# Performance work log

Hardware: AMD Instinct MI355X
Metric: run time of the kernel (lower is better)

The kernel has to match this reference:

```python
import jax, jax.numpy as jnp
import numpy as np

B, K, H, L = 50000, 32, 128, 64
KL_BETA = 0.001
LN_EPS = 1e-5


def _layernorm(x, g, b):
    m = jnp.mean(x, axis=-1, keepdims=True)
    v = jnp.mean((x - m) ** 2, axis=-1, keepdims=True)
    return (x - m) * jax.lax.rsqrt(v + LN_EPS) * g + b


def setup_inputs() -> dict:
    key = jax.random.key(0)
    ks = jax.random.split(key, 16)
    s = 0.05
    return {
        "self_feat": jax.random.normal(ks[0], (B, H), jnp.float32),
        "neighbor_feat": jax.random.normal(ks[1], (B, K, H), jnp.float32),
        "trust_mask": jax.random.uniform(ks[2], (B, K, 1), jnp.float32),
        "eps": jax.random.normal(ks[3], (B, K, L), jnp.float32),
        "pre_g": jnp.ones((H,), jnp.float32), "pre_b": jnp.zeros((H,), jnp.float32),
        "W_mu": jax.random.normal(ks[4], (H, L), jnp.float32) * s, "b_mu": jnp.zeros((L,), jnp.float32),
        "W_lv": jax.random.normal(ks[5], (H, L), jnp.float32) * s, "b_lv": jnp.zeros((L,), jnp.float32),
        "post_g": jnp.ones((L,), jnp.float32), "post_b": jnp.zeros((L,), jnp.float32),
        "W_q": jax.random.normal(ks[6], (H, L), jnp.float32) * s, "b_q": jnp.zeros((L,), jnp.float32),
        "W_k": jax.random.normal(ks[7], (L, L), jnp.float32) * s, "b_k": jnp.zeros((L,), jnp.float32),
        "W_v": jax.random.normal(ks[8], (L, L), jnp.float32) * s, "b_v": jnp.zeros((L,), jnp.float32),
        "W_o": jax.random.normal(ks[9], (L, H), jnp.float32) * s, "b_o": jnp.zeros((H,), jnp.float32),
    }


def reference(self_feat, neighbor_feat, trust_mask, eps,
              pre_g, pre_b, W_mu, b_mu, W_lv, b_lv, post_g, post_b,
              W_q, b_q, W_k, b_k, W_v, b_v, W_o, b_o):
    # [B,K,H] -> layernorm -> VIB reparameterization -> [B,K,L]
    nn = _layernorm(neighbor_feat, pre_g, pre_b)
    mu = nn @ W_mu + b_mu                      # [B,K,L]
    logvar = nn @ W_lv + b_lv                  # [B,K,L]
    z = mu + eps * jnp.exp(0.5 * logvar)       # reparam
    z = _layernorm(z, post_g, post_b)
    # trust-masked single-query attention over K neighbors
    q = self_feat @ W_q + b_q                  # [B,L]
    k = z @ W_k + b_k                          # [B,K,L]
    v = z @ W_v + b_v                          # [B,K,L]
    logits = jnp.einsum("bl,bkl->bk", q, k) / jnp.sqrt(jnp.float32(L))
    logits = logits + jnp.log(trust_mask[..., 0] + 1e-6)
    attn = jax.nn.softmax(logits, axis=-1)     # [B,K]
    context = jnp.einsum("bk,bkl->bl", attn, v)
    comm_feat = context @ W_o + b_o            # [B,H]
    kl = -0.5 * jnp.mean(jnp.sum(1.0 + logvar - mu ** 2 - jnp.exp(logvar), axis=-1))
    return comm_feat, KL_BETA * kl
```

## Files before the change

kernel.cpp:

```cpp
#include <hip/hip_runtime.h>
#include <hip/hip_bf16.h>

typedef float f32x4 __attribute__((ext_vector_type(4)));
typedef short bf16x8 __attribute__((ext_vector_type(8)));

#define NB 50000
#define NK 32
#define NH 128
#define NL 64

static __device__ __forceinline__ unsigned short f2bf(float f) {
    unsigned int u = __float_as_uint(f);
    u += 0x7fffu + ((u >> 16) & 1u);
    return (unsigned short)(u >> 16);
}
static __device__ __forceinline__ float bf2f(unsigned short u) {
    return __uint_as_float(((unsigned int)u) << 16);
}
static __device__ __forceinline__ float bflo(unsigned int u) { return __uint_as_float(u << 16); }
static __device__ __forceinline__ float bfhi(unsigned int u) { return __uint_as_float(u & 0xffff0000u); }

__global__ void kl_zero_kernel(float* out) {
    if (threadIdx.x == 0 && blockIdx.x == 0) out[(size_t)NB * NH] = 0.0f;
}

__global__ void __launch_bounds__(256) wvo_kernel(const float* __restrict__ W_v,
                                                  const float* __restrict__ W_o,
                                                  const float* __restrict__ b_v,
                                                  const float* __restrict__ b_o,
                                                  float* __restrict__ wvo_ws,
                                                  float* __restrict__ bvo_ws)
{
    const int t = threadIdx.x;
    for (int e = t; e < 64 * 128; e += 256) {
        int d = e >> 7, h = e & 127;
        float s = 0.f;
#pragma unroll 8
        for (int c = 0; c < 64; ++c) s += W_v[d * 64 + c] * W_o[c * 128 + h];
        wvo_ws[e] = s;
    }
    if (t < 128) {
        float s = b_o[t];
#pragma unroll 8
        for (int c = 0; c < 64; ++c) s += b_v[c] * W_o[c * 128 + t];
        bvo_ws[t] = s;
    }
}

__global__ void __launch_bounds__(256) qk_kernel(const float* __restrict__ self_feat,
                                                 const float* __restrict__ W_q,
                                                 const float* __restrict__ b_q,
                                                 const float* __restrict__ W_k,
                                                 float* __restrict__ qk_ws)
{
    __shared__ __align__(16) unsigned short A[32 * 128];
    __shared__ __align__(16) unsigned short ZQ[32 * 64];
    const int t = threadIdx.x, w = t >> 6, l = t & 63, g = l >> 4, li = l & 15;

    bf16x8 Bq[4];
#pragma unroll
    for (int s = 0; s < 4; ++s) {
        int k0 = 32 * s + 8 * g, c = li + 16 * w;
        bf16x8 f;
#pragma unroll
        for (int j = 0; j < 8; ++j) f[j] = (short)f2bf(W_q[(k0 + j) * 64 + c]);
        Bq[s] = f;
    }
    bf16x8 Bk[2];
#pragma unroll
    for (int s = 0; s < 2; ++s) {
        int k0 = 32 * s + 8 * g, d = li + 16 * w;
        bf16x8 f;
#pragma unroll
        for (int j = 0; j < 8; ++j) f[j] = (short)f2bf(W_k[d * 64 + k0 + j]);
        Bk[s] = f;
    }
    const float bq = b_q[li + 16 * w];
    const int n0 = blockIdx.x * 32;

    {
        int row = t >> 3, c0 = (t & 7) * 16;
        float x[16];
        if (n0 + row < NB) {
            const float* src = self_feat + (size_t)(n0 + row) * NH + c0;
#pragma unroll
            for (int i = 0; i < 4; ++i) {
                float4 v4 = ((const float4*)src)[i];
                x[4 * i] = v4.x; x[4 * i + 1] = v4.y; x[4 * i + 2] = v4.z; x[4 * i + 3] = v4.w;
            }
        } else {
#pragma unroll
            for (int i = 0; i < 16; ++i) x[i] = 0.f;
        }
        alignas(16) unsigned short yb[16];
#pragma unroll
        for (int i = 0; i < 16; ++i) yb[i] = f2bf(x[i]);
        int boff = row * 256 + c0 * 2;
        *(int4*)((char*)A + ((boff) ^ ((row & 7) << 4))) = *(int4*)&yb[0];
        *(int4*)((char*)A + ((boff + 16) ^ ((row & 7) << 4))) = *(int4*)&yb[8];
    }
    __syncthreads();

    const f32x4 zero4 = {0.f, 0.f, 0.f, 0.f};
    f32x4 acc[2] = {zero4, zero4};
#pragma unroll
    for (int s = 0; s < 4; ++s) {
        bf16x8 A0 = *(const bf16x8*)((const char*)A + ((li * 256 + s * 64 + g * 16) ^ ((li & 7) << 4)));
        bf16x8 A1 = *(const bf16x8*)((const char*)A + (((16 + li) * 256 + s * 64 + g * 16) ^ ((li & 7) << 4)));
        acc[0] = __builtin_amdgcn_mfma_f32_16x16x32_bf16(A0, Bq[s], acc[0], 0, 0, 0);
        acc[1] = __builtin_amdgcn_mfma_f32_16x16x32_bf16(A1, Bq[s], acc[1], 0, 0, 0);
    }
#pragma unroll
    for (int mt = 0; mt < 2; ++mt)
#pragma unroll
        for (int r = 0; r < 4; ++r) {
            int row = 16 * mt + 4 * g + r, c = li + 16 * w;
            *(unsigned short*)((char*)ZQ + ((row * 128 + c * 2) ^ ((row & 7) << 4))) = f2bf(acc[mt][r] + bq);
        }
    __syncthreads();

    f32x4 acc2[2] = {zero4, zero4};
#pragma unroll
    for (int s = 0; s < 2; ++s) {
        bf16x8 A0 = *(const bf16x8*)((const char*)ZQ + ((li * 128 + s * 64 + g * 16) ^ ((li & 7) << 4)));
        bf16x8 A1 = *(const bf16x8*)((const char*)ZQ + (((16 + li) * 128 + s * 64 + g * 16) ^ (((16 + li) & 7) << 4)));
        acc2[0] = __builtin_amdgcn_mfma_f32_16x16x32_bf16(A0, Bk[s], acc2[0], 0, 0, 0);
        acc2[1] = __builtin_amdgcn_mfma_f32_16x16x32_bf16(A1, Bk[s], acc2[1], 0, 0, 0);
    }
#pragma unroll
    for (int mt = 0; mt < 2; ++mt)
#pragma unroll
        for (int r = 0; r < 4; ++r) {
            int row = 16 * mt + 4 * g + r;
            if (n0 + row < NB)
                qk_ws[(size_t)(n0 + row) * 64 + li + 16 * w] = acc2[mt][r];
        }
}

__global__ void __launch_bounds__(256) fz10_kernel(
    const float* __restrict__ neighbor_feat, const float* __restrict__ trust_mask,
    const float* __restrict__ eps_g,
    const float* __restrict__ pre_g, const float* __restrict__ pre_b,
    const float* __restrict__ W_mu, const float* __restrict__ b_mu,
    const float* __restrict__ W_lv, const float* __restrict__ b_lv,
    const float* __restrict__ post_g, const float* __restrict__ post_b,
    const float* __restrict__ qk_ws, const float* __restrict__ wvo_ws,
    const float* __restrict__ bvo_ws,
    float* __restrict__ out)
{
    __shared__ __align__(16) unsigned short A[32 * 128];
    __shared__ float muv[128 * 33];
    __shared__ float2 s_pgb[128];
    __shared__ float s_bmu[64], s_blv[64], s_pg[64], s_pb[64];
    __shared__ float logit_l[32];
    __shared__ float zpart[4][64];
    __shared__ float klw[4];

    const int t = threadIdx.x, w = t >> 6, l = t & 63, g = l >> 4, li = l & 15;

    if (t < 128) s_pgb[t] = make_float2(pre_g[t], pre_b[t]);
    if (t < 64) { s_bmu[t] = b_mu[t]; s_blv[t] = b_lv[t]; s_pg[t] = post_g[t]; s_pb[t] = post_b[t]; }

    bf16x8 Wml[2][4];
    {
        const float* Wsrc = (w < 2) ? W_mu : W_lv;
        int cb = 32 * (w & 1) + li;
#pragma unroll
        for (int ntp = 0; ntp < 2; ++ntp)
#pragma unroll
            for (int s = 0; s < 4; ++s) {
                int k0 = 32 * s + 8 * g, c = cb + 16 * ntp;
                bf16x8 f;
#pragma unroll
                for (int j = 0; j < 8; ++j) f[j] = (short)f2bf(Wsrc[(k0 + j) * 64 + c]);
                Wml[ntp][s] = f;
            }
    }
    const int h = 32 * w + (l & 31);
    const int chalf = l >> 5;
    unsigned int wvo_pk[16];
#pragma unroll
    for (int j = 0; j < 16; ++j) {
        int c = 32 * chalf + 2 * j;
        wvo_pk[j] = (unsigned)f2bf(wvo_ws[c * 128 + h]) | ((unsigned)f2bf(wvo_ws[(c + 1) * 128 + h]) << 16);
    }
    const float bvo_r = bvo_ws[h];
    __syncthreads();

    const int row = t >> 3;
    const int c0 = (t & 7) * 16;
    const int l0 = (t & 7) * 8;
    int bn = blockIdx.x * 8;

    float x[16], ee[8], qk8[8], trr;
    {
        const float* src = neighbor_feat + ((size_t)bn * NK + row) * NH + c0;
#pragma unroll
        for (int i = 0; i < 4; ++i) {
            float4 v4 = ((const float4*)src)[i];
            x[4 * i] = v4.x; x[4 * i + 1] = v4.y; x[4 * i + 2] = v4.z; x[4 * i + 3] = v4.w;
        }
        const float* ep = eps_g + ((size_t)bn * NK + row) * NL + l0;
        float4 e0 = ((const float4*)ep)[0], e1 = ((const float4*)ep)[1];
        ee[0] = e0.x; ee[1] = e0.y; ee[2] = e0.z; ee[3] = e0.w;
        ee[4] = e1.x; ee[5] = e1.y; ee[6] = e1.z; ee[7] = e1.w;
        const float* qp = qk_ws + (size_t)bn * 64 + l0;
        float4 q0 = ((const float4*)qp)[0], q1 = ((const float4*)qp)[1];
        qk8[0] = q0.x; qk8[1] = q0.y; qk8[2] = q0.z; qk8[3] = q0.w;
        qk8[4] = q1.x; qk8[5] = q1.y; qk8[6] = q1.z; qk8[7] = q1.w;
        trr = trust_mask[(size_t)bn * NK + row];
    }

    float kl_acc = 0.f;
    const f32x4 zero4 = {0.f, 0.f, 0.f, 0.f};

#pragma unroll 1
    for (int i = 0; i < 8; ++i, ++bn) {
        const int bnx = (i < 7) ? bn + 1 : bn;

        float s1 = 0.f;
#pragma unroll
        for (int j = 0; j < 16; ++j) s1 += x[j];
        s1 += __shfl_xor(s1, 1); s1 += __shfl_xor(s1, 2); s1 += __shfl_xor(s1, 4);
        float mean = s1 * (1.f / 128.f);
        float s2 = 0.f;
#pragma unroll
        for (int j = 0; j < 16; ++j) { float d = x[j] - mean; s2 += d * d; }
        s2 += __shfl_xor(s2, 1); s2 += __shfl_xor(s2, 2); s2 += __shfl_xor(s2, 4);
        float inv = rsqrtf(s2 * (1.f / 128.f) + 1e-5f);
        alignas(16) unsigned short yb[16];
#pragma unroll
        for (int j = 0; j < 16; ++j) {
            float2 gb = s_pgb[c0 + j];
            yb[j] = f2bf((x[j] - mean) * inv * gb.x + gb.y);
        }
        {
            int boff = row * 256 + c0 * 2;
            *(int4*)((char*)A + ((boff) ^ ((row & 7) << 4))) = *(int4*)&yb[0];
            *(int4*)((char*)A + ((boff + 16) ^ ((row & 7) << 4))) = *(int4*)&yb[8];
        }
        {
            const float* src = neighbor_feat + ((size_t)bnx * NK + row) * NH + c0;
#pragma unroll
            for (int j = 0; j < 4; ++j) {
                float4 v4 = ((const float4*)src)[j];
                x[4 * j] = v4.x; x[4 * j + 1] = v4.y; x[4 * j + 2] = v4.z; x[4 * j + 3] = v4.w;
            }
        }
        __syncthreads();

        {
            f32x4 acc[2][2];
            acc[0][0] = zero4; acc[0][1] = zero4; acc[1][0] = zero4; acc[1][1] = zero4;
#pragma unroll
            for (int s = 0; s < 4; ++s) {
                bf16x8 A0 = *(const bf16x8*)((const char*)A + ((li * 256 + s * 64 + g * 16) ^ ((li & 7) << 4)));
                bf16x8 A1 = *(const bf16x8*)((const char*)A + (((16 + li) * 256 + s * 64 + g * 16) ^ ((li & 7) << 4)));
#pragma unroll
                for (int ntp = 0; ntp < 2; ++ntp) {
                    acc[0][ntp] = __builtin_amdgcn_mfma_f32_16x16x32_bf16(A0, Wml[ntp][s], acc[0][ntp], 0, 0, 0);
                    acc[1][ntp] = __builtin_amdgcn_mfma_f32_16x16x32_bf16(A1, Wml[ntp][s], acc[1][ntp], 0, 0, 0);
                }
            }
#pragma unroll
            for (int mt = 0; mt < 2; ++mt)
#pragma unroll
                for (int ntp = 0; ntp < 2; ++ntp)
#pragma unroll
                    for (int r = 0; r < 4; ++r)
                        muv[(32 * w + 16 * ntp + li) * 33 + (16 * mt + 4 * g + r)] = acc[mt][ntp][r];
        }
        __syncthreads();

        float zr[8];
#pragma unroll
        for (int j = 0; j < 8; ++j) {
            float mu = muv[(l0 + j) * 33 + row] + s_bmu[l0 + j];
            float lv = muv[(64 + l0 + j) * 33 + row] + s_blv[l0 + j];
            float eh = __expf(0.5f * lv);
            kl_acc += 1.f + lv - mu * mu - eh * eh;
            zr[j] = mu + ee[j] * eh;
        }
        {
            const float* ep = eps_g + ((size_t)bnx * NK + row) * NL + l0;
            float4 e0 = ((const float4*)ep)[0], e1 = ((const float4*)ep)[1];
            ee[0] = e0.x; ee[1] = e0.y; ee[2] = e0.z; ee[3] = e0.w;
            ee[4] = e1.x; ee[5] = e1.y; ee[6] = e1.z; ee[7] = e1.w;
        }
        {
            float zs = 0.f;
#pragma unroll
            for (int j = 0; j < 8; ++j) zs += zr[j];
            zs += __shfl_xor(zs, 1); zs += __shfl_xor(zs, 2); zs += __shfl_xor(zs, 4);
            float zm = zs * (1.f / 64.f);
            float zv = 0.f;
#pragma unroll
            for (int j = 0; j < 8; ++j) { float d = zr[j] - zm; zv += d * d; }
            zv += __shfl_xor(zv, 1); zv += __shfl_xor(zv, 2); zv += __shfl_xor(zv, 4);
            float zi = rsqrtf(zv * (1.f / 64.f) + 1e-5f);
#pragma unroll
            for (int j = 0; j < 8; ++j)
                zr[j] = (zr[j] - zm) * zi * s_pg[l0 + j] + s_pb[l0 + j];
        }
        {
            float lg = 0.f;
#pragma unroll
            for (int j = 0; j < 8; ++j) lg += zr[j] * qk8[j];
            lg += __shfl_xor(lg, 1); lg += __shfl_xor(lg, 2); lg += __shfl_xor(lg, 4);
            if ((t & 7) == 0) logit_l[row] = lg * 0.125f + __logf(trr + 1e-6f);
        }
        {
            const float* qp = qk_ws + (size_t)bnx * 64 + l0;
            float4 q0 = ((const float4*)qp)[0], q1 = ((const float4*)qp)[1];
            qk8[0] = q0.x; qk8[1] = q0.y; qk8[2] = q0.z; qk8[3] = q0.w;
            qk8[4] = q1.x; qk8[5] = q1.y; qk8[6] = q1.z; qk8[7] = q1.w;
            trr = trust_mask[(size_t)bnx * NK + row];
        }
        __syncthreads();

        {
            float lgv = logit_l[l & 31];
            float mx = lgv;
            mx = fmaxf(mx, __shfl_xor(mx, 1));  mx = fmaxf(mx, __shfl_xor(mx, 2));
            mx = fmaxf(mx, __shfl_xor(mx, 4));  mx = fmaxf(mx, __shfl_xor(mx, 8));
            mx = fmaxf(mx, __shfl_xor(mx, 16));
            float ev = __expf(lgv - mx);
            float den = ev;
            den += __shfl_xor(den, 1); den += __shfl_xor(den, 2);
            den += __shfl_xor(den, 4); den += __shfl_xor(den, 8);
            den += __shfl_xor(den, 16);
            float att_own = __expf(logit_l[row] - mx) / den;
            float av[8];
#pragma unroll
            for (int j = 0; j < 8; ++j) av[j] = att_own * zr[j];
#pragma unroll
            for (int j = 0; j < 8; ++j) {
                av[j] += __shfl_xor(av[j], 8);
                av[j] += __shfl_xor(av[j], 16);
                av[j] += __shfl_xor(av[j], 32);
            }
            if (l < 8) {
                float4 p0 = {av[0], av[1], av[2], av[3]};
                float4 p1 = {av[4], av[5], av[6], av[7]};
                ((float4*)&zpart[w][8 * l])[0] = p0;
                ((float4*)&zpart[w][8 * l])[1] = p1;
            }
        }
        __syncthreads();

        {
            float o = 0.f;
#pragma unroll
            for (int j = 0; j < 16; ++j) {
                int c = 32 * chalf + 2 * j;
                float2 z0 = *(const float2*)&zpart[0][c];
                float2 z1 = *(const float2*)&zpart[1][c];
                float2 z2 = *(const float2*)&zpart[2][c];
                float2 z3 = *(const float2*)&zpart[3][c];
                float zs0 = z0.x + z1.x + z2.x + z3.x;
                float zs1 = z0.y + z1.y + z2.y + z3.y;
                o += zs0 * bflo(wvo_pk[j]) + zs1 * bfhi(wvo_pk[j]);
            }
            o += __shfl_xor(o, 32);
            if (l < 32) out[(size_t)bn * NH + h] = o + bvo_r;
        }
    }

#pragma unroll
    for (int msk = 1; msk < 64; msk <<= 1) kl_acc += __shfl_xor(kl_acc, msk);
    if (l == 0) klw[w] = kl_acc;
    __syncthreads();
    if (t == 0) {
        float tot = klw[0] + klw[1] + klw[2] + klw[3];
        atomicAdd(out + (size_t)NB * NH, tot * (-0.5f * 0.001f / ((float)NB * NK)));
    }
}

extern "C" void kernel_launch(void* const* d_in, const int* in_sizes, int n_in,
                              void* d_out, int out_size, void* d_ws, size_t ws_size,
                              hipStream_t stream) {
    const float* self_feat     = (const float*)d_in[0];
    const float* neighbor_feat = (const float*)d_in[1];
    const float* trust_mask    = (const float*)d_in[2];
    const float* eps           = (const float*)d_in[3];
    const float* pre_g  = (const float*)d_in[4];
    const float* pre_b  = (const float*)d_in[5];
    const float* W_mu   = (const float*)d_in[6];
    const float* b_mu   = (const float*)d_in[7];
    const float* W_lv   = (const float*)d_in[8];
    const float* b_lv   = (const float*)d_in[9];
    const float* post_g = (const float*)d_in[10];
    const float* post_b = (const float*)d_in[11];
    const float* W_q    = (const float*)d_in[12];
    const float* b_q    = (const float*)d_in[13];
    const float* W_k    = (const float*)d_in[14];
    const float* W_v    = (const float*)d_in[16];
    const float* b_v    = (const float*)d_in[17];
    const float* W_o    = (const float*)d_in[18];
    const float* b_o    = (const float*)d_in[19];
    float* out = (float*)d_out;

    float* qk_ws  = (float*)d_ws;
    float* wvo_ws = qk_ws + (size_t)NB * 64;
    float* bvo_ws = wvo_ws + 64 * 128;

    hipLaunchKernelGGL(kl_zero_kernel, dim3(1), dim3(64), 0, stream, out);
    hipLaunchKernelGGL(wvo_kernel, dim3(1), dim3(256), 0, stream, W_v, W_o, b_v, b_o, wvo_ws, bvo_ws);
    hipLaunchKernelGGL(qk_kernel, dim3((NB + 31) / 32), dim3(256), 0, stream,
                       self_feat, W_q, b_q, W_k, qk_ws);
    hipLaunchKernelGGL(fz10_kernel, dim3(NB / 8), dim3(256), 0, stream,
                       neighbor_feat, trust_mask, eps, pre_g, pre_b,
                       W_mu, b_mu, W_lv, b_lv, post_g, post_b,
                       qk_ws, wvo_ws, bvo_ws, out);
}
```

Before: 522.1 us.

## Batch output projection across 8 rows via MFMA and reorganize muv layout

The per-row output projection (context @ W_vo) with its extra __syncthreads per iteration is replaced by accumulating all 8 rows' context vectors in shared memory and doing one batched MFMA at the end. A split hi/lo bf16 trick keeps the activations near fp32 precision. The muv shared buffer is transposed to a row-major layout with 132 padding, and the lane-to-column mapping switches from contiguous to strided so eps/qk loads become scalar and strided. This removes one barrier per loop iteration but wastes half the MFMA rows and makes the eps/qk global loads less vectorized.

```diff
diff --git a/kernel.cpp b/kernel.cpp
--- a/kernel.cpp
+++ b/kernel.cpp
@@ -17,8 +17,6 @@
 static __device__ __forceinline__ float bf2f(unsigned short u) {
     return __uint_as_float(((unsigned int)u) << 16);
 }
-static __device__ __forceinline__ float bflo(unsigned int u) { return __uint_as_float(u << 16); }
-static __device__ __forceinline__ float bfhi(unsigned int u) { return __uint_as_float(u & 0xffff0000u); }
 
 __global__ void kl_zero_kernel(float* out) {
     if (threadIdx.x == 0 && blockIdx.x == 0) out[(size_t)NB * NH] = 0.0f;
@@ -137,7 +135,7 @@
         }
 }
 
-__global__ void __launch_bounds__(256) fz10_kernel(
+__global__ void __launch_bounds__(256) fz11_kernel(
     const float* __restrict__ neighbor_feat, const float* __restrict__ trust_mask,
     const float* __restrict__ eps_g,
     const float* __restrict__ pre_g, const float* __restrict__ pre_b,
@@ -149,11 +147,11 @@
     float* __restrict__ out)
 {
     __shared__ __align__(16) unsigned short A[32 * 128];
-    __shared__ float muv[128 * 33];
+    __shared__ float muv[32 * 132];
+    __shared__ float zparts[8][4][64];
     __shared__ float2 s_pgb[128];
     __shared__ float s_bmu[64], s_blv[64], s_pg[64], s_pb[64];
     __shared__ float logit_l[32];
-    __shared__ float zpart[4][64];
     __shared__ float klw[4];
 
     const int t = threadIdx.x, w = t >> 6, l = t & 63, g = l >> 4, li = l & 15;
@@ -176,21 +174,25 @@
                 Wml[ntp][s] = f;
             }
     }
-    const int h = 32 * w + (l & 31);
-    const int chalf = l >> 5;
-    unsigned int wvo_pk[16];
-#pragma unroll
-    for (int j = 0; j < 16; ++j) {
-        int c = 32 * chalf + 2 * j;
-        wvo_pk[j] = (unsigned)f2bf(wvo_ws[c * 128 + h]) | ((unsigned)f2bf(wvo_ws[(c + 1) * 128 + h]) << 16);
-    }
-    const float bvo_r = bvo_ws[h];
+    bf16x8 Bvo[2][2];
+#pragma unroll
+    for (int nt = 0; nt < 2; ++nt)
+#pragma unroll
+        for (int s = 0; s < 2; ++s) {
+            int k0 = 32 * s + 8 * g, c = 32 * w + 16 * nt + li;
+            bf16x8 f;
+#pragma unroll
+            for (int j = 0; j < 8; ++j) f[j] = (short)f2bf(wvo_ws[(k0 + j) * 128 + c]);
+            Bvo[nt][s] = f;
+        }
+    const float bvo2[2] = { bvo_ws[32 * w + li], bvo_ws[32 * w + 16 + li] };
     __syncthreads();
 
     const int row = t >> 3;
     const int c0 = (t & 7) * 16;
-    const int l0 = (t & 7) * 8;
-    int bn = blockIdx.x * 8;
+    const int a  = t & 7;
+    const int bn0 = blockIdx.x * 8;
+    int bn = bn0;
 
     float x[16], ee[8], qk8[8], trr;
     {
@@ -200,14 +202,10 @@
             float4 v4 = ((const float4*)src)[i];
             x[4 * i] = v4.x; x[4 * i + 1] = v4.y; x[4 * i + 2] = v4.z; x[4 * i + 3] = v4.w;
         }
-        const float* ep = eps_g + ((size_t)bn * NK + row) * NL + l0;
-        float4 e0 = ((const float4*)ep)[0], e1 = ((const float4*)ep)[1];
-        ee[0] = e0.x; ee[1] = e0.y; ee[2] = e0.z; ee[3] = e0.w;
-        ee[4] = e1.x; ee[5] = e1.y; ee[6] = e1.z; ee[7] = e1.w;
-        const float* qp = qk_ws + (size_t)bn * 64 + l0;
-        float4 q0 = ((const float4*)qp)[0], q1 = ((const float4*)qp)[1];
-        qk8[0] = q0.x; qk8[1] = q0.y; qk8[2] = q0.z; qk8[3] = q0.w;
-        qk8[4] = q1.x; qk8[5] = q1.y; qk8[6] = q1.z; qk8[7] = q1.w;
+        const float* ep = eps_g + ((size_t)bn * NK + row) * NL;
+        const float* qp = qk_ws + (size_t)bn * 64;
+#pragma unroll
+        for (int j = 0; j < 8; ++j) { ee[j] = ep[a + 8 * j]; qk8[j] = qp[a + 8 * j]; }
         trr = trust_mask[(size_t)bn * NK + row];
     }
 
@@ -268,24 +266,24 @@
                 for (int ntp = 0; ntp < 2; ++ntp)
 #pragma unroll
                     for (int r = 0; r < 4; ++r)
-                        muv[(32 * w + 16 * ntp + li) * 33 + (16 * mt + 4 * g + r)] = acc[mt][ntp][r];
+                        muv[(16 * mt + 4 * g + r) * 132 + 32 * w + 16 * ntp + li] = acc[mt][ntp][r];
         }
         __syncthreads();
 
         float zr[8];
 #pragma unroll
         for (int j = 0; j < 8; ++j) {
-            float mu = muv[(l0 + j) * 33 + row] + s_bmu[l0 + j];
-            float lv = muv[(64 + l0 + j) * 33 + row] + s_blv[l0 + j];
+            int c = a + 8 * j;
+            float mu = muv[row * 132 + c] + s_bmu[c];
+            float lv = muv[row * 132 + 64 + c] + s_blv[c];
             float eh = __expf(0.5f * lv);
             kl_acc += 1.f + lv - mu * mu - eh * eh;
             zr[j] = mu + ee[j] * eh;
         }
         {
-            const float* ep = eps_g + ((size_t)bnx * NK + row) * NL + l0;
-            float4 e0 = ((const float4*)ep)[0], e1 = ((const float4*)ep)[1];
-            ee[0] = e0.x; ee[1] = e0.y; ee[2] = e0.z; ee[3] = e0.w;
-            ee[4] = e1.x; ee[5] = e1.y; ee[6] = e1.z; ee[7] = e1.w;
+            const float* ep = eps_g + ((size_t)bnx * NK + row) * NL;
+#pragma unroll
+            for (int j = 0; j < 8; ++j) ee[j] = ep[a + 8 * j];
         }
         {
             float zs = 0.f;
@@ -299,21 +297,22 @@
             zv += __shfl_xor(zv, 1); zv += __shfl_xor(zv, 2); zv += __shfl_xor(zv, 4);
             float zi = rsqrtf(zv * (1.f / 64.f) + 1e-5f);
 #pragma unroll
-            for (int j = 0; j < 8; ++j)
-                zr[j] = (zr[j] - zm) * zi * s_pg[l0 + j] + s_pb[l0 + j];
+            for (int j = 0; j < 8; ++j) {
+                int c = a + 8 * j;
+                zr[j] = (zr[j] - zm) * zi * s_pg[c] + s_pb[c];
+            }
         }
         {
             float lg = 0.f;
 #pragma unroll
             for (int j = 0; j < 8; ++j) lg += zr[j] * qk8[j];
             lg += __shfl_xor(lg, 1); lg += __shfl_xor(lg, 2); lg += __shfl_xor(lg, 4);
-            if ((t & 7) == 0) logit_l[row] = lg * 0.125f + __logf(trr + 1e-6f);
-        }
-        {
-            const float* qp = qk_ws + (size_t)bnx * 64 + l0;
-            float4 q0 = ((const float4*)qp)[0], q1 = ((const float4*)qp)[1];
-            qk8[0] = q0.x; qk8[1] = q0.y; qk8[2] = q0.z; qk8[3] = q0.w;
-            qk8[4] = q1.x; qk8[5] = q1.y; qk8[6] = q1.z; qk8[7] = q1.w;
+            if (a == 0) logit_l[row] = lg * 0.125f + __logf(trr + 1e-6f);
+        }
+        {
+            const float* qp = qk_ws + (size_t)bnx * 64;
+#pragma unroll
+            for (int j = 0; j < 8; ++j) qk8[j] = qp[a + 8 * j];
             trr = trust_mask[(size_t)bnx * NK + row];
         }
         __syncthreads();
@@ -340,30 +339,44 @@
                 av[j] += __shfl_xor(av[j], 32);
             }
             if (l < 8) {
-                float4 p0 = {av[0], av[1], av[2], av[3]};
-                float4 p1 = {av[4], av[5], av[6], av[7]};
-                ((float4*)&zpart[w][8 * l])[0] = p0;
-                ((float4*)&zpart[w][8 * l])[1] = p1;
-            }
-        }
-        __syncthreads();
-
-        {
-            float o = 0.f;
-#pragma unroll
-            for (int j = 0; j < 16; ++j) {
-                int c = 32 * chalf + 2 * j;
-                float2 z0 = *(const float2*)&zpart[0][c];
-                float2 z1 = *(const float2*)&zpart[1][c];
-                float2 z2 = *(const float2*)&zpart[2][c];
-                float2 z3 = *(const float2*)&zpart[3][c];
-                float zs0 = z0.x + z1.x + z2.x + z3.x;
-                float zs1 = z0.y + z1.y + z2.y + z3.y;
-                o += zs0 * bflo(wvo_pk[j]) + zs1 * bfhi(wvo_pk[j]);
-            }
-            o += __shfl_xor(o, 32);
-            if (l < 32) out[(size_t)bn * NH + h] = o + bvo_r;
-        }
+#pragma unroll
+                for (int j = 0; j < 8; ++j) zparts[i][w][l + 8 * j] = av[j];
+            }
+        }
+    }
+    __syncthreads();
+
+    {
+        bf16x8 Ahi[2], Alo[2];
+#pragma unroll
+        for (int s = 0; s < 2; ++s)
+#pragma unroll
+            for (int j = 0; j < 8; ++j) {
+                float z = 0.f;
+                if (li < 8) {
+                    int c = 32 * s + 8 * g + j;
+                    z = zparts[li][0][c] + zparts[li][1][c] + zparts[li][2][c] + zparts[li][3][c];
+                }
+                unsigned short hi = f2bf(z);
+                Ahi[s][j] = (short)hi;
+                Alo[s][j] = (short)f2bf(z - bf2f(hi));
+            }
+        f32x4 accE[2] = {zero4, zero4};
+#pragma unroll
+        for (int s = 0; s < 2; ++s)
+#pragma unroll
+            for (int nt = 0; nt < 2; ++nt) {
+                accE[nt] = __builtin_amdgcn_mfma_f32_16x16x32_bf16(Ahi[s], Bvo[nt][s], accE[nt], 0, 0, 0);
+                accE[nt] = __builtin_amdgcn_mfma_f32_16x16x32_bf16(Alo[s], Bvo[nt][s], accE[nt], 0, 0, 0);
+            }
+#pragma unroll
+        for (int nt = 0; nt < 2; ++nt)
+#pragma unroll
+            for (int r = 0; r < 4; ++r) {
+                int rr = 4 * g + r;
+                if (rr < 8)
+                    out[(size_t)(bn0 + rr) * NH + 32 * w + 16 * nt + li] = accE[nt][r] + bvo2[nt];
+            }
     }
 
 #pragma unroll
@@ -408,7 +421,7 @@
     hipLaunchKernelGGL(wvo_kernel, dim3(1), dim3(256), 0, stream, W_v, W_o, b_v, b_o, wvo_ws, bvo_ws);
     hipLaunchKernelGGL(qk_kernel, dim3((NB + 31) / 32), dim3(256), 0, stream,
                        self_feat, W_q, b_q, W_k, qk_ws);
-    hipLaunchKernelGGL(fz10_kernel, dim3(NB / 8), dim3(256), 0, stream,
+    hipLaunchKernelGGL(fz11_kernel, dim3(NB / 8), dim3(256), 0, stream,
                        neighbor_feat, trust_mask, eps, pre_g, pre_b,
                        W_mu, b_mu, W_lv, b_lv, post_g, post_b,
                        qk_ws, wvo_ws, bvo_ws, out);
```

New measurement: 508.5 us. 2.6% less time.
